# Kernel optimization log

Hardware: AMD Instinct MI355X
Metric: run time of the kernel (lower is better)

The kernel has to match this reference:

```python
import jax, jax.numpy as jnp
import numpy as np

Q_HEADS, KV_HEADS, HEAD_SIZE, H, MAX_LEN = 16, 4, 64, 1024, 4096
B, S = 1, 4096


def _rope_tables(max_len, head_size):
    half = head_size // 2
    inv_freq = 1.0 / (10000.0 ** (np.arange(half, dtype=np.float32) / half))
    pos = np.arange(max_len, dtype=np.float32)
    ang = pos[:, None] * inv_freq[None, :]  # [max_len, half]
    return jnp.asarray(np.sin(ang)), jnp.asarray(np.cos(ang))


def setup_inputs() -> dict:
    key = jax.random.key(0)
    ks = jax.random.split(key, 6)
    sc = 1.0 / np.sqrt(H)
    x = jax.random.normal(ks[0], (B, S, H), dtype=jnp.float32)
    wq = jax.random.normal(ks[1], (H, H), dtype=jnp.float32) * sc
    wk = jax.random.normal(ks[2], (H, KV_HEADS * HEAD_SIZE), dtype=jnp.float32) * sc
    wv = jax.random.normal(ks[3], (H, KV_HEADS * HEAD_SIZE), dtype=jnp.float32) * sc
    wo = jax.random.normal(ks[4], (H, H), dtype=jnp.float32) * sc
    sin, cos = _rope_tables(MAX_LEN, HEAD_SIZE)
    full_mask = jnp.tril(jnp.ones((MAX_LEN, MAX_LEN), dtype=bool))
    attention_mask = jnp.ones((B, S), dtype=jnp.int32)
    return {"x": x, "attention_mask": attention_mask, "start": 0,
            "wq": wq, "wk": wk, "wv": wv, "wo": wo,
            "sin": sin, "cos": cos, "full_mask": full_mask}


def _rotate(t, sin, cos, start):
    # t: [b, heads, s, head_size]; interleaved even/odd RoPE
    s = t.shape[2]
    sn = sin[start:start + s, :][None, None, :, :]
    cs = cos[start:start + s, :][None, None, :, :]
    even, odd = t[..., 0::2], t[..., 1::2]
    out_even = cs * even - sn * odd
    out_odd = sn * even + cs * odd
    return jnp.stack((out_even, out_odd), axis=-1).reshape(t.shape)


def _expand_kv(t, group):
    # [b, kv_heads, s, d] -> [b, kv_heads*group, s, d]
    b, kvh, s, d = t.shape
    return jnp.broadcast_to(t[:, :, None], (b, kvh, group, s, d)).reshape(b, kvh * group, s, d)


def reference(x, attention_mask, start, wq, wk, wv, wo, sin, cos, full_mask):
    b, s, _ = x.shape
    group = Q_HEADS // KV_HEADS
    Q = (x @ wq).reshape(b, s, Q_HEADS, HEAD_SIZE).transpose(0, 2, 1, 3)
    K = (x @ wk).reshape(b, s, KV_HEADS, HEAD_SIZE).transpose(0, 2, 1, 3)
    V = (x @ wv).reshape(b, s, KV_HEADS, HEAD_SIZE).transpose(0, 2, 1, 3)
    Q = _rotate(Q, sin, cos, start)
    K = _rotate(K, sin, cos, start)
    K = _expand_kv(K, group)
    V = _expand_kv(V, group)
    z = jnp.einsum('bhqd,bhkd->bhqk', Q, K) / (HEAD_SIZE ** 0.5)
    kv_len = start + s
    mask = full_mask[:s, :kv_len][None, None, :, :]
    amask = (attention_mask[:, :kv_len] != 0)[:, None, None, :]
    mask = mask & amask
    z = jnp.where(mask, z, -1000000.0)
    A = jax.nn.softmax(z, axis=-1)
    ctx = jnp.einsum('bhqk,bhkd->bhqd', A, V)
    q_mask = attention_mask[:, :s].astype(ctx.dtype)[:, None, :, None]
    ctx = ctx * q_mask
    ctx = ctx.transpose(0, 2, 1, 3).reshape(b, s, H)
    return ctx @ wo
```

## Files before the change

### kernel.cpp

```cpp
#include <hip/hip_runtime.h>

typedef __bf16 bf16x8 __attribute__((ext_vector_type(8)));
typedef float f32x4 __attribute__((ext_vector_type(4)));
typedef unsigned int u32x4 __attribute__((ext_vector_type(4)));

typedef const void __attribute__((address_space(1)))* gas1;
typedef void __attribute__((address_space(3)))* las3;

__device__ __forceinline__ unsigned short f2bf(float f) {
  unsigned int u = __builtin_bit_cast(unsigned int, f);
  u += 0x7fffu + ((u >> 16) & 1u);
  return (unsigned short)(u >> 16);
}
__device__ __forceinline__ float bf2f(unsigned short h) {
  unsigned int u = ((unsigned int)h) << 16;
  return __builtin_bit_cast(float, u);
}
__device__ __forceinline__ unsigned int pack2bf(float lo, float hi) {
  return (unsigned int)f2bf(lo) | ((unsigned int)f2bf(hi) << 16);
}
__device__ __forceinline__ unsigned int packtr(float lo, float hi) {
  return __builtin_amdgcn_perm(__builtin_bit_cast(unsigned int, hi),
                               __builtin_bit_cast(unsigned int, lo), 0x07060302u);
}

__global__ __launch_bounds__(256) void prep(const float* __restrict__ x,
                                            const float* __restrict__ wq,
                                            const float* __restrict__ wk,
                                            const float* __restrict__ wv,
                                            const float* __restrict__ wo,
                                            unsigned short* __restrict__ xb,
                                            unsigned short* __restrict__ wtqkv,
                                            unsigned short* __restrict__ wot) {
  __shared__ float tile[32][33];
  const int b = blockIdx.x;
  const int tid = threadIdx.x;
  if (b < 4096) {
    int i = b * 256 + tid;
    float4 v = ((const float4*)x)[i];
    uint2 o;
    o.x = pack2bf(v.x, v.y);
    o.y = pack2bf(v.z, v.w);
    ((uint2*)xb)[i] = o;
    return;
  }
  const float* src;
  unsigned short* dst;
  int R, C, t;
  if (b < 5120)      { t = b - 4096; src = wq; dst = wtqkv;               R = 1024; C = 1024; }
  else if (b < 5376) { t = b - 5120; src = wk; dst = wtqkv + 1024 * 1024; R = 1024; C = 256; }
  else if (b < 5632) { t = b - 5376; src = wv; dst = wtqkv + 1280 * 1024; R = 1024; C = 256; }
  else               { t = b - 5632; src = wo; dst = wot;                 R = 1024; C = 1024; }
  const int ntc = C >> 5;
  const int c0 = (t % ntc) * 32, r0 = (t / ntc) * 32;
  const int tx = tid & 31, ty = tid >> 5;
#pragma unroll
  for (int i = 0; i < 4; ++i)
    tile[ty + i * 8][tx] = src[(r0 + ty + i * 8) * C + c0 + tx];
  __syncthreads();
#pragma unroll
  for (int i = 0; i < 4; ++i)
    dst[(c0 + ty + i * 8) * R + r0 + tx] = f2bf(tile[tx][ty + i * 8]);
}

__global__ __launch_bounds__(256, 2) void gemm_bt2(const unsigned short* __restrict__ A,
                                                   const unsigned short* __restrict__ Bt,
                                                   void* __restrict__ Cout,
                                                   int M, int N, int K, int outF32) {
  __shared__ __align__(16) unsigned short Als[128 * 32];
  __shared__ __align__(16) unsigned short Bls[128 * 32];
  const int tid = threadIdx.x;
  const int wave = tid >> 6, lane = tid & 63;
  const int lgrp = lane >> 4, lmod = lane & 15;
  const int wm = (wave & 1) * 64, wn = (wave >> 1) * 64;
  const int m0 = blockIdx.y * 128, n0 = blockIdx.x * 128;

  f32x4 acc[4][4] = {};

  for (int k0 = 0; k0 < K; k0 += 32) {
    __syncthreads();
#pragma unroll
    for (int it = 0; it < 2; ++it) {
      int idx = tid + it * 256;
      int rr = idx >> 2, cc = (idx & 3) * 8;
      __builtin_amdgcn_global_load_lds((gas1)(const void*)&A[(size_t)(m0 + rr) * K + k0 + cc],
                                       (las3)(void*)&Als[(it * 256 + wave * 64) * 8], 16, 0, 0);
      __builtin_amdgcn_global_load_lds((gas1)(const void*)&Bt[(size_t)(n0 + rr) * K + k0 + cc],
                                       (las3)(void*)&Bls[(it * 256 + wave * 64) * 8], 16, 0, 0);
    }
    __syncthreads();
    bf16x8 af[4], bfr[4];
#pragma unroll
    for (int mi = 0; mi < 4; ++mi)
      af[mi] = __builtin_bit_cast(bf16x8, *(const u32x4*)&Als[(wm + mi * 16 + lmod) * 32 + lgrp * 8]);
#pragma unroll
    for (int ni = 0; ni < 4; ++ni)
      bfr[ni] = __builtin_bit_cast(bf16x8, *(const u32x4*)&Bls[(wn + ni * 16 + lmod) * 32 + lgrp * 8]);
#pragma unroll
    for (int mi = 0; mi < 4; ++mi)
#pragma unroll
      for (int ni = 0; ni < 4; ++ni)
        acc[mi][ni] = __builtin_amdgcn_mfma_f32_16x16x32_bf16(af[mi], bfr[ni], acc[mi][ni], 0, 0, 0);
  }

#pragma unroll
  for (int mi = 0; mi < 4; ++mi)
#pragma unroll
    for (int ni = 0; ni < 4; ++ni)
#pragma unroll
      for (int r = 0; r < 4; ++r) {
        int row = m0 + wm + mi * 16 + lgrp * 4 + r;
        int col = n0 + wn + ni * 16 + lmod;
        float v = acc[mi][ni][r];
        if (outF32) ((float*)Cout)[(size_t)row * N + col] = v;
        else ((unsigned short*)Cout)[(size_t)row * N + col] = f2bf(v);
      }
}

__global__ __launch_bounds__(256) void rope_vt(const unsigned short* __restrict__ qkv,
                                               const float* __restrict__ sinT,
                                               const float* __restrict__ cosT,
                                               unsigned short* __restrict__ Qh,
                                               unsigned short* __restrict__ Kh,
                                               unsigned short* __restrict__ Vt) {
  __shared__ unsigned short tile[32][33];
  const int b = blockIdx.x;
  const int tid = threadIdx.x;
  if (b < 5120) {
    const float qscale = 0.18033688011112042f;
    int u = b * 256 + tid;
    int s = u / 320, cu = u % 320;
    int col = cu * 4;
    uint2 pr = *(const uint2*)&qkv[s * 1536 + col];
    float e0 = bf2f((unsigned short)(pr.x & 0xffff));
    float o0 = bf2f((unsigned short)(pr.x >> 16));
    float e1 = bf2f((unsigned short)(pr.y & 0xffff));
    float o1 = bf2f((unsigned short)(pr.y >> 16));
    if (col < 1024) {
      int h = col >> 6, d = col & 63, i0 = d >> 1;
      float sn0 = sinT[s * 32 + i0], cs0 = cosT[s * 32 + i0];
      float sn1 = sinT[s * 32 + i0 + 1], cs1 = cosT[s * 32 + i0 + 1];
      uint2 w;
      w.x = pack2bf((cs0 * e0 - sn0 * o0) * qscale, (sn0 * e0 + cs0 * o0) * qscale);
      w.y = pack2bf((cs1 * e1 - sn1 * o1) * qscale, (sn1 * e1 + cs1 * o1) * qscale);
      *(uint2*)&Qh[(h * 4096 + s) * 64 + d] = w;
    } else {
      int c = col - 1024;
      int h = c >> 6, d = c & 63, i0 = d >> 1;
      float sn0 = sinT[s * 32 + i0], cs0 = cosT[s * 32 + i0];
      float sn1 = sinT[s * 32 + i0 + 1], cs1 = cosT[s * 32 + i0 + 1];
      uint2 w;
      w.x = pack2bf(cs0 * e0 - sn0 * o0, sn0 * e0 + cs0 * o0);
      w.y = pack2bf(cs1 * e1 - sn1 * o1, sn1 * e1 + cs1 * o1);
      *(uint2*)&Kh[(h * 4096 + s) * 64 + d] = w;
    }
    return;
  }
  int t = b - 5120;
  int h = t >> 8, rem = t & 255;
  int d0 = (rem >> 7) * 32, s0 = (rem & 127) * 32;
  int tx = tid & 31, ty = tid >> 5;
#pragma unroll
  for (int i = 0; i < 4; ++i)
    tile[ty + i * 8][tx] = qkv[(s0 + ty + i * 8) * 1536 + 1280 + h * 64 + d0 + tx];
  __syncthreads();
#pragma unroll
  for (int i = 0; i < 4; ++i)
    Vt[(h * 64 + d0 + ty + i * 8) * 4096 + s0 + tx] = tile[tx][ty + i * 8];
}

__global__ __launch_bounds__(256, 2) void attn3(const unsigned short* __restrict__ Qh,
                                                const unsigned short* __restrict__ Kh,
                                                const unsigned short* __restrict__ Vt,
                                                unsigned short* __restrict__ ctx) {
  __shared__ __align__(16) unsigned short Kls[128 * 68];
  __shared__ __align__(16) unsigned short Vls[64 * 136];
  const int bx = blockIdx.x;
  const int head = bx & 15;
  const int qidx = bx >> 4;
  const int qb = (qidx < 16) ? (31 - qidx) : (qidx - 16);
  const int kvh = head >> 2;
  const int tid = threadIdx.x;
  const int wave = tid >> 6, lane = tid & 63;
  const int lgrp = lane >> 4, lmod = lane & 15;
  const int qbase = qb * 128;

  const unsigned short* Kg = Kh + (size_t)kvh * 4096 * 64;
  const unsigned short* Vg = Vt + (size_t)kvh * 64 * 4096;

  bf16x8 qf[2][2];
  int qrow[2];
#pragma unroll
  for (int qt = 0; qt < 2; ++qt) {
    qrow[qt] = qbase + wave * 32 + qt * 16 + lmod;
    const unsigned short* Qg = Qh + ((size_t)head * 4096 + qrow[qt]) * 64;
    qf[qt][0] = __builtin_bit_cast(bf16x8, *(const u32x4*)&Qg[lgrp * 8]);
    qf[qt][1] = __builtin_bit_cast(bf16x8, *(const u32x4*)&Qg[32 + lgrp * 8]);
  }

  const int kbase = (8 * (lmod >> 2) + (lmod & 3)) * 68 + lgrp * 8;
  const int vbase = lmod * 136 + lgrp * 8;

  f32x4 accO[2][4] = {};
  float m_i[2] = {-3e38f, -3e38f}, l_i[2] = {0.f, 0.f};

  for (int kc = 0; kc <= qb; ++kc) {
    const int kb = kc * 128;
    __syncthreads();
#pragma unroll
    for (int i = 0; i < 4; ++i) {
      int ii = tid + i * 256;
      int r = ii >> 3, sg = (ii & 7) * 8;
      u32x4 dK = *(const u32x4*)&Kg[(size_t)(kb + r) * 64 + sg];
      uint2* pd = (uint2*)&Kls[r * 68 + sg];
      pd[0] = make_uint2(dK[0], dK[1]);
      pd[1] = make_uint2(dK[2], dK[3]);
    }
#pragma unroll
    for (int i = 0; i < 4; ++i) {
      int ii = tid + i * 256;
      int r = ii >> 4, sg = (ii & 15) * 8;
      *(u32x4*)&Vls[r * 136 + sg] = *(const u32x4*)&Vg[(size_t)r * 4096 + kb + sg];
    }
    __syncthreads();

    f32x4 s[4][2][2];
#pragma unroll
    for (int g = 0; g < 4; ++g)
#pragma unroll
      for (int t = 0; t < 2; ++t) {
        const unsigned short* ka = &Kls[kbase + (32 * g + 4 * t) * 68];
        uint2 a0 = *(const uint2*)&ka[0];
        uint2 a1 = *(const uint2*)&ka[4];
        uint2 b0 = *(const uint2*)&ka[32];
        uint2 b1 = *(const uint2*)&ka[36];
        u32x4 lo = {a0.x, a0.y, a1.x, a1.y};
        u32x4 hi = {b0.x, b0.y, b1.x, b1.y};
        bf16x8 alo = __builtin_bit_cast(bf16x8, lo);
        bf16x8 ahi = __builtin_bit_cast(bf16x8, hi);
#pragma unroll
        for (int qt = 0; qt < 2; ++qt) {
          f32x4 z = {};
          z = __builtin_amdgcn_mfma_f32_16x16x32_bf16(alo, qf[qt][0], z, 0, 0, 0);
          z = __builtin_amdgcn_mfma_f32_16x16x32_bf16(ahi, qf[qt][1], z, 0, 0, 0);
          s[g][t][qt] = z;
        }
      }

#pragma unroll
    for (int qt = 0; qt < 2; ++qt) {
      if (kb + 127 > qbase + wave * 32 + qt * 16) {
#pragma unroll
        for (int g = 0; g < 4; ++g)
#pragma unroll
          for (int t = 0; t < 2; ++t)
#pragma unroll
            for (int r = 0; r < 4; ++r) {
              int key = kb + 32 * g + 8 * lgrp + 4 * t + r;
              if (key > qrow[qt]) s[g][t][qt][r] = -3e38f;
            }
      }
    }

#pragma unroll
    for (int qt = 0; qt < 2; ++qt) {
      f32x4 v0 = s[0][0][qt], v1 = s[0][1][qt];
#pragma unroll
      for (int g = 1; g < 4; ++g)
#pragma unroll
        for (int r = 0; r < 4; ++r) {
          v0[r] = fmaxf(v0[r], s[g][0][qt][r]);
          v1[r] = fmaxf(v1[r], s[g][1][qt][r]);
        }
      float mx = fmaxf(fmaxf(fmaxf(v0[0], v0[1]), fmaxf(v0[2], v0[3])),
                       fmaxf(fmaxf(v1[0], v1[1]), fmaxf(v1[2], v1[3])));
      mx = fmaxf(mx, __shfl_xor(mx, 16, 64));
      mx = fmaxf(mx, __shfl_xor(mx, 32, 64));
      float mnew = fmaxf(m_i[qt], mx);
      float alpha = __builtin_amdgcn_exp2f(m_i[qt] - mnew);
      m_i[qt] = mnew;
      f32x4 su = {};
#pragma unroll
      for (int g = 0; g < 4; ++g)
#pragma unroll
        for (int t = 0; t < 2; ++t)
#pragma unroll
          for (int r = 0; r < 4; ++r) {
            float ev = __builtin_amdgcn_exp2f(s[g][t][qt][r] - mnew);
            s[g][t][qt][r] = ev;
            su[r] += ev;
          }
      float rs = (su[0] + su[1]) + (su[2] + su[3]);
      rs += __shfl_xor(rs, 16, 64);
      rs += __shfl_xor(rs, 32, 64);
      l_i[qt] = l_i[qt] * alpha + rs;
#pragma unroll
      for (int dt = 0; dt < 4; ++dt)
#pragma unroll
        for (int r = 0; r < 4; ++r) accO[qt][dt][r] *= alpha;
    }

#pragma unroll
    for (int g = 0; g < 4; ++g) {
      bf16x8 pf[2];
#pragma unroll
      for (int qt = 0; qt < 2; ++qt) {
        u32x4 pk;
        pk[0] = packtr(s[g][0][qt][0], s[g][0][qt][1]);
        pk[1] = packtr(s[g][0][qt][2], s[g][0][qt][3]);
        pk[2] = packtr(s[g][1][qt][0], s[g][1][qt][1]);
        pk[3] = packtr(s[g][1][qt][2], s[g][1][qt][3]);
        pf[qt] = __builtin_bit_cast(bf16x8, pk);
      }
#pragma unroll
      for (int dt = 0; dt < 4; ++dt) {
        bf16x8 vf = __builtin_bit_cast(bf16x8, *(const u32x4*)&Vls[vbase + dt * 2176 + 32 * g]);
        accO[0][dt] = __builtin_amdgcn_mfma_f32_16x16x32_bf16(vf, pf[0], accO[0][dt], 0, 0, 0);
        accO[1][dt] = __builtin_amdgcn_mfma_f32_16x16x32_bf16(vf, pf[1], accO[1][dt], 0, 0, 0);
      }
    }
  }

#pragma unroll
  for (int qt = 0; qt < 2; ++qt) {
    float inv = 1.f / l_i[qt];
#pragma unroll
    for (int dt = 0; dt < 4; ++dt) {
      uint2 o;
      o.x = pack2bf(accO[qt][dt][0] * inv, accO[qt][dt][1] * inv);
      o.y = pack2bf(accO[qt][dt][2] * inv, accO[qt][dt][3] * inv);
      *(uint2*)&ctx[(size_t)qrow[qt] * 1024 + head * 64 + dt * 16 + lgrp * 4] = o;
    }
  }
}

extern "C" void kernel_launch(void* const* d_in, const int* in_sizes, int n_in,
                              void* d_out, int out_size, void* d_ws, size_t ws_size,
                              hipStream_t stream) {
  const float* x    = (const float*)d_in[0];
  const float* wq   = (const float*)d_in[3];
  const float* wk   = (const float*)d_in[4];
  const float* wv   = (const float*)d_in[5];
  const float* wo   = (const float*)d_in[6];
  const float* sinT = (const float*)d_in[7];
  const float* cosT = (const float*)d_in[8];

  unsigned short* ws    = (unsigned short*)d_ws;
  unsigned short* xb    = ws;
  unsigned short* wtqkv = xb + 4096 * 1024;
  unsigned short* wot   = wtqkv + 1536 * 1024;
  unsigned short* qkv   = wot + 1024 * 1024;
  unsigned short* Qh    = qkv + 4096 * 1536;
  unsigned short* Kh    = Qh + 16 * 4096 * 64;
  unsigned short* Vt    = Kh + 4 * 4096 * 64;
  unsigned short* ctx   = Vt + 4 * 64 * 4096;
  float* out = (float*)d_out;

  prep<<<6656, 256, 0, stream>>>(x, wq, wk, wv, wo, xb, wtqkv, wot);
  gemm_bt2<<<dim3(12, 32), 256, 0, stream>>>(xb, wtqkv, qkv, 4096, 1536, 1024, 0);
  rope_vt<<<6144, 256, 0, stream>>>(qkv, sinT, cosT, Qh, Kh, Vt);
  attn3<<<dim3(512), 256, 0, stream>>>(Qh, Kh, Vt, ctx);
  gemm_bt2<<<dim3(8, 32), 256, 0, stream>>>(ctx, wot, out, 4096, 1024, 1024, 1);
}
```

Measured before the change: 258.1 us.

## Fuse RoPE and V transpose into QKV GEMM epilogue, swizzle K tile in attention

The QKV projection GEMM now applies RoPE (with the Q scale) in its epilogue and writes Q, K and transposed V directly. This removes the separate rope_vt kernel and the round trip of the intermediate qkv buffer. The GEMM K-loop now stages 64-wide K per barrier pair to halve synchronisations, which doubles LDS use. The attention kernel stores K in LDS with an XOR-swizzled layout so each fragment is a single 16-byte read instead of four 8-byte reads. The epilogue writes become scattered bf16 stores, and the rotation pairs are exchanged with shuffles.

```diff
diff --git a/kernel.cpp b/kernel.cpp
--- a/kernel.cpp
+++ b/kernel.cpp
@@ -63,12 +63,16 @@
     dst[(c0 + ty + i * 8) * R + r0 + tx] = f2bf(tile[tx][ty + i * 8]);
 }
 
-__global__ __launch_bounds__(256, 2) void gemm_bt2(const unsigned short* __restrict__ A,
+__global__ __launch_bounds__(256, 2) void gemm_qkv(const unsigned short* __restrict__ A,
                                                    const unsigned short* __restrict__ Bt,
-                                                   void* __restrict__ Cout,
-                                                   int M, int N, int K, int outF32) {
-  __shared__ __align__(16) unsigned short Als[128 * 32];
-  __shared__ __align__(16) unsigned short Bls[128 * 32];
+                                                   const float* __restrict__ sinT,
+                                                   const float* __restrict__ cosT,
+                                                   unsigned short* __restrict__ Qh,
+                                                   unsigned short* __restrict__ Kh,
+                                                   unsigned short* __restrict__ Vt) {
+  __shared__ __align__(16) unsigned short Als[2][128 * 32];
+  __shared__ __align__(16) unsigned short Bls[2][128 * 32];
+  const int K = 1024;
   const int tid = threadIdx.x;
   const int wave = tid >> 6, lane = tid & 63;
   const int lgrp = lane >> 4, lmod = lane & 15;
@@ -77,30 +81,138 @@
 
   f32x4 acc[4][4] = {};
 
-  for (int k0 = 0; k0 < K; k0 += 32) {
-    __syncthreads();
-#pragma unroll
-    for (int it = 0; it < 2; ++it) {
-      int idx = tid + it * 256;
-      int rr = idx >> 2, cc = (idx & 3) * 8;
-      __builtin_amdgcn_global_load_lds((gas1)(const void*)&A[(size_t)(m0 + rr) * K + k0 + cc],
-                                       (las3)(void*)&Als[(it * 256 + wave * 64) * 8], 16, 0, 0);
-      __builtin_amdgcn_global_load_lds((gas1)(const void*)&Bt[(size_t)(n0 + rr) * K + k0 + cc],
-                                       (las3)(void*)&Bls[(it * 256 + wave * 64) * 8], 16, 0, 0);
-    }
-    __syncthreads();
-    bf16x8 af[4], bfr[4];
+  for (int k0 = 0; k0 < K; k0 += 64) {
+    __syncthreads();
+#pragma unroll
+    for (int half = 0; half < 2; ++half) {
+      int kk = k0 + half * 32;
+#pragma unroll
+      for (int it = 0; it < 2; ++it) {
+        int idx = tid + it * 256;
+        int rr = idx >> 2, cc = (idx & 3) * 8;
+        __builtin_amdgcn_global_load_lds((gas1)(const void*)&A[(size_t)(m0 + rr) * K + kk + cc],
+                                         (las3)(void*)&Als[half][(it * 256 + wave * 64) * 8], 16, 0, 0);
+        __builtin_amdgcn_global_load_lds((gas1)(const void*)&Bt[(size_t)(n0 + rr) * K + kk + cc],
+                                         (las3)(void*)&Bls[half][(it * 256 + wave * 64) * 8], 16, 0, 0);
+      }
+    }
+    __syncthreads();
+#pragma unroll
+    for (int half = 0; half < 2; ++half) {
+      bf16x8 af[4], bfr[4];
+#pragma unroll
+      for (int mi = 0; mi < 4; ++mi)
+        af[mi] = __builtin_bit_cast(bf16x8, *(const u32x4*)&Als[half][(wm + mi * 16 + lmod) * 32 + lgrp * 8]);
+#pragma unroll
+      for (int ni = 0; ni < 4; ++ni)
+        bfr[ni] = __builtin_bit_cast(bf16x8, *(const u32x4*)&Bls[half][(wn + ni * 16 + lmod) * 32 + lgrp * 8]);
+#pragma unroll
+      for (int mi = 0; mi < 4; ++mi)
+#pragma unroll
+        for (int ni = 0; ni < 4; ++ni)
+          acc[mi][ni] = __builtin_amdgcn_mfma_f32_16x16x32_bf16(af[mi], bfr[ni], acc[mi][ni], 0, 0, 0);
+    }
+  }
+
+  const int cbase = n0 + wn;
+  if (cbase >= 1280) {
+    const int kvh = (cbase - 1280) >> 6;
 #pragma unroll
     for (int mi = 0; mi < 4; ++mi)
-      af[mi] = __builtin_bit_cast(bf16x8, *(const u32x4*)&Als[(wm + mi * 16 + lmod) * 32 + lgrp * 8]);
-#pragma unroll
-    for (int ni = 0; ni < 4; ++ni)
-      bfr[ni] = __builtin_bit_cast(bf16x8, *(const u32x4*)&Bls[(wn + ni * 16 + lmod) * 32 + lgrp * 8]);
-#pragma unroll
-    for (int mi = 0; mi < 4; ++mi)
+#pragma unroll
+      for (int ni = 0; ni < 4; ++ni) {
+        int d = ni * 16 + lmod;
+        int s = m0 + wm + mi * 16 + lgrp * 4;
+        uint2 o;
+        o.x = pack2bf(acc[mi][ni][0], acc[mi][ni][1]);
+        o.y = pack2bf(acc[mi][ni][2], acc[mi][ni][3]);
+        *(uint2*)&Vt[((size_t)(kvh * 64 + d)) * 4096 + s] = o;
+      }
+    return;
+  }
+
+  __syncthreads();
+  float* sinls = (float*)&Als[0][0];
+  float* cosls = (float*)&Bls[0][0];
+#pragma unroll
+  for (int j = 0; j < 4; ++j) {
+    int idx = tid + j * 256;
+    int rr = idx >> 3, cc = (idx & 7) * 4;
+    *(float4*)&sinls[rr * 32 + cc] = *(const float4*)&sinT[(size_t)(m0 + rr) * 32 + cc];
+    *(float4*)&cosls[rr * 32 + cc] = *(const float4*)&cosT[(size_t)(m0 + rr) * 32 + cc];
+  }
+  __syncthreads();
+
+  const float qscale = 0.18033688011112042f;
+  const bool isQ = (cbase < 1024);
+  const int h = isQ ? (cbase >> 6) : ((cbase - 1024) >> 6);
+  unsigned short* dstbase = isQ ? Qh : Kh;
+  const bool evn = (lmod & 1) == 0;
+#pragma unroll
+  for (int mi = 0; mi < 4; ++mi)
+#pragma unroll
+    for (int ni = 0; ni < 4; ++ni) {
+      int d = ni * 16 + lmod;
+      int i = ni * 8 + (lmod >> 1);
+#pragma unroll
+      for (int r = 0; r < 4; ++r) {
+        float v = acc[mi][ni][r];
+        float p = __shfl_xor(v, 1, 64);
+        int rl = wm + mi * 16 + lgrp * 4 + r;
+        float sn = sinls[rl * 32 + i], cs = cosls[rl * 32 + i];
+        float e = evn ? v : p, o = evn ? p : v;
+        float outv = evn ? (cs * e - sn * o) : (sn * e + cs * o);
+        if (isQ) outv *= qscale;
+        dstbase[((size_t)h * 4096 + m0 + rl) * 64 + d] = f2bf(outv);
+      }
+    }
+}
+
+__global__ __launch_bounds__(256, 2) void gemm_out(const unsigned short* __restrict__ A,
+                                                   const unsigned short* __restrict__ Bt,
+                                                   float* __restrict__ Cout) {
+  __shared__ __align__(16) unsigned short Als[2][128 * 32];
+  __shared__ __align__(16) unsigned short Bls[2][128 * 32];
+  const int K = 1024, N = 1024;
+  const int tid = threadIdx.x;
+  const int wave = tid >> 6, lane = tid & 63;
+  const int lgrp = lane >> 4, lmod = lane & 15;
+  const int wm = (wave & 1) * 64, wn = (wave >> 1) * 64;
+  const int m0 = blockIdx.y * 128, n0 = blockIdx.x * 128;
+
+  f32x4 acc[4][4] = {};
+
+  for (int k0 = 0; k0 < K; k0 += 64) {
+    __syncthreads();
+#pragma unroll
+    for (int half = 0; half < 2; ++half) {
+      int kk = k0 + half * 32;
+#pragma unroll
+      for (int it = 0; it < 2; ++it) {
+        int idx = tid + it * 256;
+        int rr = idx >> 2, cc = (idx & 3) * 8;
+        __builtin_amdgcn_global_load_lds((gas1)(const void*)&A[(size_t)(m0 + rr) * K + kk + cc],
+                                         (las3)(void*)&Als[half][(it * 256 + wave * 64) * 8], 16, 0, 0);
+        __builtin_amdgcn_global_load_lds((gas1)(const void*)&Bt[(size_t)(n0 + rr) * K + kk + cc],
+                                         (las3)(void*)&Bls[half][(it * 256 + wave * 64) * 8], 16, 0, 0);
+      }
+    }
+    __syncthreads();
+#pragma unroll
+    for (int half = 0; half < 2; ++half) {
+      bf16x8 af[4], bfr[4];
+#pragma unroll
+      for (int mi = 0; mi < 4; ++mi)
+        af[mi] = __builtin_bit_cast(bf16x8, *(const u32x4*)&Als[half][(wm + mi * 16 + lmod) * 32 + lgrp * 8]);
 #pragma unroll
       for (int ni = 0; ni < 4; ++ni)
-        acc[mi][ni] = __builtin_amdgcn_mfma_f32_16x16x32_bf16(af[mi], bfr[ni], acc[mi][ni], 0, 0, 0);
+        bfr[ni] = __builtin_bit_cast(bf16x8, *(const u32x4*)&Bls[half][(wn + ni * 16 + lmod) * 32 + lgrp * 8]);
+#pragma unroll
+      for (int mi = 0; mi < 4; ++mi)
+#pragma unroll
+        for (int ni = 0; ni < 4; ++ni)
+          acc[mi][ni] = __builtin_amdgcn_mfma_f32_16x16x32_bf16(af[mi], bfr[ni], acc[mi][ni], 0, 0, 0);
+    }
   }
 
 #pragma unroll
@@ -111,69 +223,15 @@
       for (int r = 0; r < 4; ++r) {
         int row = m0 + wm + mi * 16 + lgrp * 4 + r;
         int col = n0 + wn + ni * 16 + lmod;
-        float v = acc[mi][ni][r];
-        if (outF32) ((float*)Cout)[(size_t)row * N + col] = v;
-        else ((unsigned short*)Cout)[(size_t)row * N + col] = f2bf(v);
-      }
-}
-
-__global__ __launch_bounds__(256) void rope_vt(const unsigned short* __restrict__ qkv,
-                                               const float* __restrict__ sinT,
-                                               const float* __restrict__ cosT,
-                                               unsigned short* __restrict__ Qh,
-                                               unsigned short* __restrict__ Kh,
-                                               unsigned short* __restrict__ Vt) {
-  __shared__ unsigned short tile[32][33];
-  const int b = blockIdx.x;
-  const int tid = threadIdx.x;
-  if (b < 5120) {
-    const float qscale = 0.18033688011112042f;
-    int u = b * 256 + tid;
-    int s = u / 320, cu = u % 320;
-    int col = cu * 4;
-    uint2 pr = *(const uint2*)&qkv[s * 1536 + col];
-    float e0 = bf2f((unsigned short)(pr.x & 0xffff));
-    float o0 = bf2f((unsigned short)(pr.x >> 16));
-    float e1 = bf2f((unsigned short)(pr.y & 0xffff));
-    float o1 = bf2f((unsigned short)(pr.y >> 16));
-    if (col < 1024) {
-      int h = col >> 6, d = col & 63, i0 = d >> 1;
-      float sn0 = sinT[s * 32 + i0], cs0 = cosT[s * 32 + i0];
-      float sn1 = sinT[s * 32 + i0 + 1], cs1 = cosT[s * 32 + i0 + 1];
-      uint2 w;
-      w.x = pack2bf((cs0 * e0 - sn0 * o0) * qscale, (sn0 * e0 + cs0 * o0) * qscale);
-      w.y = pack2bf((cs1 * e1 - sn1 * o1) * qscale, (sn1 * e1 + cs1 * o1) * qscale);
-      *(uint2*)&Qh[(h * 4096 + s) * 64 + d] = w;
-    } else {
-      int c = col - 1024;
-      int h = c >> 6, d = c & 63, i0 = d >> 1;
-      float sn0 = sinT[s * 32 + i0], cs0 = cosT[s * 32 + i0];
-      float sn1 = sinT[s * 32 + i0 + 1], cs1 = cosT[s * 32 + i0 + 1];
-      uint2 w;
-      w.x = pack2bf(cs0 * e0 - sn0 * o0, sn0 * e0 + cs0 * o0);
-      w.y = pack2bf(cs1 * e1 - sn1 * o1, sn1 * e1 + cs1 * o1);
-      *(uint2*)&Kh[(h * 4096 + s) * 64 + d] = w;
-    }
-    return;
-  }
-  int t = b - 5120;
-  int h = t >> 8, rem = t & 255;
-  int d0 = (rem >> 7) * 32, s0 = (rem & 127) * 32;
-  int tx = tid & 31, ty = tid >> 5;
-#pragma unroll
-  for (int i = 0; i < 4; ++i)
-    tile[ty + i * 8][tx] = qkv[(s0 + ty + i * 8) * 1536 + 1280 + h * 64 + d0 + tx];
-  __syncthreads();
-#pragma unroll
-  for (int i = 0; i < 4; ++i)
-    Vt[(h * 64 + d0 + ty + i * 8) * 4096 + s0 + tx] = tile[tx][ty + i * 8];
-}
-
-__global__ __launch_bounds__(256, 2) void attn3(const unsigned short* __restrict__ Qh,
+        Cout[(size_t)row * N + col] = acc[mi][ni][r];
+      }
+}
+
+__global__ __launch_bounds__(256, 2) void attn5(const unsigned short* __restrict__ Qh,
                                                 const unsigned short* __restrict__ Kh,
                                                 const unsigned short* __restrict__ Vt,
                                                 unsigned short* __restrict__ ctx) {
-  __shared__ __align__(16) unsigned short Kls[128 * 68];
+  __shared__ __align__(16) unsigned short Kls[8 * 128 * 8];
   __shared__ __align__(16) unsigned short Vls[64 * 136];
   const int bx = blockIdx.x;
   const int head = bx & 15;
@@ -198,7 +256,10 @@
     qf[qt][1] = __builtin_bit_cast(bf16x8, *(const u32x4*)&Qg[32 + lgrp * 8]);
   }
 
-  const int kbase = (8 * (lmod >> 2) + (lmod & 3)) * 68 + lgrp * 8;
+  int krd[2];
+#pragma unroll
+  for (int h = 0; h < 2; ++h)
+    krd[h] = (h * 64 + lgrp * 16 + (lmod ^ (h * 4 + lgrp))) * 8;
   const int vbase = lmod * 136 + lgrp * 8;
 
   f32x4 accO[2][4] = {};
@@ -210,11 +271,13 @@
 #pragma unroll
     for (int i = 0; i < 4; ++i) {
       int ii = tid + i * 256;
-      int r = ii >> 3, sg = (ii & 7) * 8;
-      u32x4 dK = *(const u32x4*)&Kg[(size_t)(kb + r) * 64 + sg];
-      uint2* pd = (uint2*)&Kls[r * 68 + sg];
-      pd[0] = make_uint2(dK[0], dK[1]);
-      pd[1] = make_uint2(dK[2], dK[3]);
+      int r = ii >> 3, s8 = ii & 7;
+      u32x4 dK = *(const u32x4*)&Kg[(size_t)(kb + r) * 64 + s8 * 8];
+      int g = r >> 5, r5 = r & 31;
+      int t = (r5 >> 2) & 1;
+      int m = ((r5 >> 3) << 2) | (r5 & 3);
+      int sigma = ((s8 >> 2) << 6) | ((s8 & 3) << 4) | (m ^ s8);
+      *(u32x4*)&Kls[(((g << 1) | t) << 10) + (sigma << 3)] = dK;
     }
 #pragma unroll
     for (int i = 0; i < 4; ++i) {
@@ -229,15 +292,9 @@
     for (int g = 0; g < 4; ++g)
 #pragma unroll
       for (int t = 0; t < 2; ++t) {
-        const unsigned short* ka = &Kls[kbase + (32 * g + 4 * t) * 68];
-        uint2 a0 = *(const uint2*)&ka[0];
-        uint2 a1 = *(const uint2*)&ka[4];
-        uint2 b0 = *(const uint2*)&ka[32];
-        uint2 b1 = *(const uint2*)&ka[36];
-        u32x4 lo = {a0.x, a0.y, a1.x, a1.y};
-        u32x4 hi = {b0.x, b0.y, b1.x, b1.y};
-        bf16x8 alo = __builtin_bit_cast(bf16x8, lo);
-        bf16x8 ahi = __builtin_bit_cast(bf16x8, hi);
+        int tb = ((g << 1) | t) << 10;
+        bf16x8 alo = __builtin_bit_cast(bf16x8, *(const u32x4*)&Kls[tb + krd[0]]);
+        bf16x8 ahi = __builtin_bit_cast(bf16x8, *(const u32x4*)&Kls[tb + krd[1]]);
 #pragma unroll
         for (int qt = 0; qt < 2; ++qt) {
           f32x4 z = {};
@@ -349,16 +406,14 @@
   unsigned short* xb    = ws;
   unsigned short* wtqkv = xb + 4096 * 1024;
   unsigned short* wot   = wtqkv + 1536 * 1024;
-  unsigned short* qkv   = wot + 1024 * 1024;
-  unsigned short* Qh    = qkv + 4096 * 1536;
+  unsigned short* Qh    = wot + 1024 * 1024;
   unsigned short* Kh    = Qh + 16 * 4096 * 64;
   unsigned short* Vt    = Kh + 4 * 4096 * 64;
   unsigned short* ctx   = Vt + 4 * 64 * 4096;
   float* out = (float*)d_out;
 
   prep<<<6656, 256, 0, stream>>>(x, wq, wk, wv, wo, xb, wtqkv, wot);
-  gemm_bt2<<<dim3(12, 32), 256, 0, stream>>>(xb, wtqkv, qkv, 4096, 1536, 1024, 0);
-  rope_vt<<<6144, 256, 0, stream>>>(qkv, sinT, cosT, Qh, Kh, Vt);
-  attn3<<<dim3(512), 256, 0, stream>>>(Qh, Kh, Vt, ctx);
-  gemm_bt2<<<dim3(8, 32), 256, 0, stream>>>(ctx, wot, out, 4096, 1024, 1024, 1);
-}
+  gemm_qkv<<<dim3(12, 32), 256, 0, stream>>>(xb, wtqkv, sinT, cosT, Qh, Kh, Vt);
+  attn5<<<dim3(512), 256, 0, stream>>>(Qh, Kh, Vt, ctx);
+  gemm_out<<<dim3(8, 32), 256, 0, stream>>>(ctx, wot, out);
+}
```

Measured after the change: 251.0 us. 2.7% less time.
